# Optimization experiments

Hardware: AMD Instinct MI355X
Metric: run time of the kernel (lower is better)

## Reference

```python
import jax, jax.numpy as jnp
import numpy as np

N, C, H, W = 4, 256, 64, 64
OC = C // 8  # reduction=8

def setup_inputs() -> dict:
    key = jax.random.key(0)
    ks = jax.random.split(key, 5)
    return {
        "x": jax.random.normal(ks[0], (N, C, H, W), jnp.float32),
        "w1": jax.random.normal(ks[1], (OC, C), jnp.float32) * 0.05,
        "w2": jax.random.normal(ks[2], (OC, C), jnp.float32) * 0.05,
        "wv": jax.random.normal(ks[3], (C, C), jnp.float32) * 0.05,
        "scale": jax.random.normal(ks[4], (1,), jnp.float32),
    }

def reference(x, w1, w2, wv, scale):
    n, c, h, w = x.shape
    hw = h * w
    xf = x.reshape(n, c, hw)                      # (n, c, hw)
    r1 = jnp.einsum('oc,nci->noi', w1, xf)        # (n, oc, hw)  conv_reduce1
    r2 = jnp.einsum('oc,nci->noi', w2, xf)        # (n, oc, hw)  conv_reduce2
    # reduce_1^T @ reduce_2 -> (n, hw, hw); softmax over last dim (dim=2)
    A = jax.nn.softmax(jnp.einsum('noi,noj->nij', r1, r2), axis=2)
    v = jnp.einsum('oc,nci->noi', wv, xf)         # (n, c, hw)   value proj
    attn = jnp.einsum('nci,nij->ncj', v, A)       # (n, c, hw)
    return x + (scale[0] * attn).reshape(n, c, h, w)
```

## Files before the change

### kernel.cpp

```cpp
#include <hip/hip_runtime.h>
#include <math.h>

#define HW    4096
#define NCH   256
#define NB    4
#define L2E   1.44269504088896340736f

typedef __attribute__((ext_vector_type(8))) short short8b;
typedef __attribute__((ext_vector_type(4))) float f32x4;

__device__ __forceinline__ unsigned short f2bf(float f) {
    unsigned int u = __float_as_uint(f);
    u += 0x7FFFu + ((u >> 16) & 1u);
    return (unsigned short)(u >> 16);
}
__device__ __forceinline__ float bf2f(unsigned short h) {
    return __uint_as_float(((unsigned int)h) << 16);
}
__device__ __forceinline__ unsigned int cvtpk_bf16(float a, float b) {
    unsigned int r;
    asm("v_cvt_pk_bf16_f32 %0, %1, %2" : "=v"(r) : "v"(a), "v"(b));
    return r;
}


__global__ __launch_bounds__(256) void proj_rr_kernel(
    const float* __restrict__ x, const float* __restrict__ w1,
    const float* __restrict__ w2,
    unsigned short* __restrict__ r1h, unsigned short* __restrict__ r1l,
    unsigned short* __restrict__ r2h, unsigned short* __restrict__ r2l)
{
    __shared__ float aT[16][36];
    __shared__ float bS[16][68];

    const int t  = threadIdx.x;
    const int i0 = blockIdx.x * 64;
    const int mh = blockIdx.y * 32;
    const int n  = blockIdx.z;

    const int tm = t >> 4;
    const int ti = t & 15;

    const int ar = t >> 3;
    const int ak = (t & 7) * 2;
    const int gm = mh + ar;
    const float* arow = (gm < 32) ? (w1 + (size_t)gm * NCH)
                                  : (w2 + (size_t)(gm - 32) * NCH);
    const float* xb = x + (size_t)n * NCH * HW;

    float acc[2][4] = {};

    for (int kc = 0; kc < NCH; kc += 16) {
        float2 av = *reinterpret_cast<const float2*>(arow + kc + ak);
        float4 bv = *reinterpret_cast<const float4*>(
            xb + (size_t)(kc + (t >> 4)) * HW + i0 + (t & 15) * 4);
        __syncthreads();
        aT[ak + 0][ar] = av.x;
        aT[ak + 1][ar] = av.y;
        *reinterpret_cast<float4*>(&bS[t >> 4][(t & 15) * 4]) = bv;
        __syncthreads();
        #pragma unroll
        for (int kk = 0; kk < 16; ++kk) {
            float2 a2 = *reinterpret_cast<const float2*>(&aT[kk][tm * 2]);
            float4 b4 = *reinterpret_cast<const float4*>(&bS[kk][ti * 4]);
            float a[2] = {a2.x, a2.y};
            float b[4] = {b4.x, b4.y, b4.z, b4.w};
            #pragma unroll
            for (int mm = 0; mm < 2; ++mm)
                #pragma unroll
                for (int jj = 0; jj < 4; ++jj)
                    acc[mm][jj] = fmaf(a[mm], b[jj], acc[mm][jj]);
        }
    }

    #pragma unroll
    for (int mm = 0; mm < 2; ++mm) {
        const int m = mh + tm * 2 + mm;
        unsigned short* bhp = (m < 32) ? r1h : r2h;
        unsigned short* blp = (m < 32) ? r1l : r2l;
        const int o = m & 31;
        #pragma unroll
        for (int jj = 0; jj < 4; ++jj) {
            const int i = i0 + ti * 4 + jj;
            float v = acc[mm][jj];
            unsigned short h = f2bf(v);
            unsigned short lo = f2bf(v - bf2f(h));
            size_t idx = ((size_t)n * HW + i) * 32 + o;
            bhp[idx] = h;
            blp[idx] = lo;
        }
    }
}

__global__ __launch_bounds__(256) void wvb_kernel(
    const float* __restrict__ wv, unsigned short* __restrict__ wvb)
{
    const int q = (blockIdx.x * 256 + threadIdx.x) * 8;
    float4 a = *reinterpret_cast<const float4*>(wv + q);
    float4 b = *reinterpret_cast<const float4*>(wv + q + 4);
    short8b o;
    o[0] = (short)f2bf(a.x); o[1] = (short)f2bf(a.y);
    o[2] = (short)f2bf(a.z); o[3] = (short)f2bf(a.w);
    o[4] = (short)f2bf(b.x); o[5] = (short)f2bf(b.y);
    o[6] = (short)f2bf(b.z); o[7] = (short)f2bf(b.w);
    *reinterpret_cast<short8b*>(wvb + q) = o;
}

__global__ __launch_bounds__(256) void proj_v_kernel(
    const float* __restrict__ x, const unsigned short* __restrict__ wvb,
    unsigned short* __restrict__ vtb)
{
    __shared__ unsigned short xt[64][40];

    const int t = threadIdx.x;
    const int w = t >> 6, l = t & 63;
    const int lj = l & 15, lg = l >> 4;
    const int iB = blockIdx.x * 64;
    const int cB = blockIdx.y * 64;
    const int n  = blockIdx.z;
    const float* xb = x + (size_t)n * NCH * HW;

    const int iw = (w >> 1) * 32;
    const int cw = (w & 1) * 32;

    f32x4 acc[2][2] = {};

    const int kr = t >> 4;
    const int ic = (t & 15) * 4;

    for (int kc = 0; kc < NCH; kc += 32) {
        float4 x0 = *reinterpret_cast<const float4*>(
            xb + (size_t)(kc + kr) * HW + iB + ic);
        float4 x1 = *reinterpret_cast<const float4*>(
            xb + (size_t)(kc + kr + 16) * HW + iB + ic);
        __syncthreads();
        xt[ic + 0][kr] = f2bf(x0.x); xt[ic + 1][kr] = f2bf(x0.y);
        xt[ic + 2][kr] = f2bf(x0.z); xt[ic + 3][kr] = f2bf(x0.w);
        xt[ic + 0][kr + 16] = f2bf(x1.x); xt[ic + 1][kr + 16] = f2bf(x1.y);
        xt[ic + 2][kr + 16] = f2bf(x1.z); xt[ic + 3][kr + 16] = f2bf(x1.w);
        __syncthreads();

        short8b xa[2], wb[2];
        #pragma unroll
        for (int is = 0; is < 2; ++is)
            xa[is] = *reinterpret_cast<const short8b*>(&xt[iw + is * 16 + lj][lg * 8]);
        #pragma unroll
        for (int cs = 0; cs < 2; ++cs)
            wb[cs] = *reinterpret_cast<const short8b*>(
                wvb + (size_t)(cB + cw + cs * 16 + lj) * NCH + kc + lg * 8);
        #pragma unroll
        for (int is = 0; is < 2; ++is)
            #pragma unroll
            for (int cs = 0; cs < 2; ++cs)
                acc[is][cs] = __builtin_amdgcn_mfma_f32_16x16x32_bf16(
                    xa[is], wb[cs], acc[is][cs], 0, 0, 0);
    }

    unsigned short* op = vtb + (size_t)n * HW * 256;
    #pragma unroll
    for (int is = 0; is < 2; ++is) {
        #pragma unroll
        for (int cs = 0; cs < 2; ++cs) {
            const int c = cB + cw + cs * 16 + lj;
            #pragma unroll
            for (int r = 0; r < 4; ++r) {
                const int i = iB + iw + is * 16 + lg * 4 + r;
                op[(size_t)(i >> 5) * 8192 + c * 32 + (i & 31)] =
                    f2bf(acc[is][cs][r]);
            }
        }
    }
}

__global__ __launch_bounds__(256) void stats_kernel(
    const unsigned short* __restrict__ r1h, const unsigned short* __restrict__ r1l,
    const unsigned short* __restrict__ r2h, const unsigned short* __restrict__ r2l,
    float* __restrict__ mpart, float* __restrict__ lpart)
{
    const int t = threadIdx.x;
    const int w = t >> 6, l = t & 63;
    const int lj = l & 15, lg = l >> 4;
    const int i0 = blockIdx.x * 64 + w * 16;
    const int jh = blockIdx.y * 1024;
    const int n  = blockIdx.z;
    const size_t nHW = (size_t)n * HW;

    const size_t ab = (nHW + i0 + lj) * 32 + lg * 8;
    const short8b ah = *reinterpret_cast<const short8b*>(r1h + ab);
    const short8b al = *reinterpret_cast<const short8b*>(r1l + ab);
    const size_t bbase = (nHW + jh + lj) * 32 + lg * 8;

    f32x4 mx = {-INFINITY, -INFINITY, -INFINITY, -INFINITY};
    {
        short8b bh = *reinterpret_cast<const short8b*>(r2h + bbase);
        for (int jt = 0; jt < 64; ++jt) {
            short8b nh = bh;
            if (jt < 63)
                nh = *reinterpret_cast<const short8b*>(r2h + bbase + (size_t)(jt + 1) * 512);
            f32x4 s = {0.f, 0.f, 0.f, 0.f};
            s = __builtin_amdgcn_mfma_f32_16x16x32_bf16(ah, bh, s, 0, 0, 0);
            #pragma unroll
            for (int r = 0; r < 4; ++r) mx[r] = fmaxf(mx[r], s[r]);
            bh = nh;
        }
    }
    #pragma unroll
    for (int msk = 1; msk < 16; msk <<= 1)
        #pragma unroll
        for (int r = 0; r < 4; ++r)
            mx[r] = fmaxf(mx[r], __shfl_xor(mx[r], msk, 64));

    f32x4 sm = {0.f, 0.f, 0.f, 0.f};
    {
        short8b bh = *reinterpret_cast<const short8b*>(r2h + bbase);
        short8b bl = *reinterpret_cast<const short8b*>(r2l + bbase);
        for (int jt = 0; jt < 64; ++jt) {
            short8b nh = bh, nl = bl;
            if (jt < 63) {
                nh = *reinterpret_cast<const short8b*>(r2h + bbase + (size_t)(jt + 1) * 512);
                nl = *reinterpret_cast<const short8b*>(r2l + bbase + (size_t)(jt + 1) * 512);
            }
            f32x4 s = {0.f, 0.f, 0.f, 0.f};
            s = __builtin_amdgcn_mfma_f32_16x16x32_bf16(al, bh, s, 0, 0, 0);
            s = __builtin_amdgcn_mfma_f32_16x16x32_bf16(ah, bl, s, 0, 0, 0);
            s = __builtin_amdgcn_mfma_f32_16x16x32_bf16(ah, bh, s, 0, 0, 0);
            #pragma unroll
            for (int r = 0; r < 4; ++r) sm[r] += __expf(s[r] - mx[r]);
            bh = nh; bl = nl;
        }
    }
    #pragma unroll
    for (int msk = 1; msk < 16; msk <<= 1)
        #pragma unroll
        for (int r = 0; r < 4; ++r)
            sm[r] += __shfl_xor(sm[r], msk, 64);

    if (lj == 0) {
        float* mp = mpart + ((size_t)blockIdx.y * NB + n) * HW + i0 + lg * 4;
        float* lp = lpart + ((size_t)blockIdx.y * NB + n) * HW + i0 + lg * 4;
        #pragma unroll
        for (int r = 0; r < 4; ++r) { mp[r] = mx[r]; lp[r] = sm[r]; }
    }
}

__global__ __launch_bounds__(256) void merge_kernel(
    const float* __restrict__ mpart, const float* __restrict__ lpart,
    float* __restrict__ ebuf)
{
    const int q = blockIdx.x * 256 + threadIdx.x;
    const int T = NB * HW;
    float m0 = mpart[q], m1 = mpart[T + q];
    float m2 = mpart[2 * T + q], m3 = mpart[3 * T + q];
    float m = fmaxf(fmaxf(m0, m1), fmaxf(m2, m3));
    float lsum = lpart[q]         * __expf(m0 - m)
               + lpart[T + q]     * __expf(m1 - m)
               + lpart[2 * T + q] * __expf(m2 - m)
               + lpart[3 * T + q] * __expf(m3 - m);
    ebuf[q] = -m * L2E - log2f(lsum);
}

__global__ __launch_bounds__(512) void attn_kernel(
    const unsigned short* __restrict__ r1h, const unsigned short* __restrict__ r1l,
    const unsigned short* __restrict__ r2h, const unsigned short* __restrict__ r2l,
    const float* __restrict__ ebuf, const unsigned short* __restrict__ vtb,
    const float* __restrict__ x, const float* __restrict__ scale,
    float* __restrict__ out)
{
    __shared__ char pl[2][4096];

    const int t = threadIdx.x;
    const int w = t >> 6, l = t & 63;
    const int lj = l & 15, lg = l >> 4;

    const int bid = blockIdx.x;
    const int xcd = bid & 7;
    const int n   = xcd >> 1;
    const int j0  = ((xcd & 1) * 64 + (bid >> 3)) * 32;
    const size_t nHW = (size_t)n * HW;

    const int iw = w & 3;
    const int jw = w >> 2;

    const size_t rb = (nHW + j0 + jw * 16 + lj) * 32 + lg * 8;
    const short8b bh = *reinterpret_cast<const short8b*>(r2h + rb);
    const short8b bl = *reinterpret_cast<const short8b*>(r2l + rb);

    const unsigned short* vtn = vtb + nHW * 256;
    const int swz = (lj & 7) << 4;
    const int wroff = (jw * 16 + lj) * 128 + ((iw * 32 + lg * 8) ^ swz);
    int rdo[2][2];
    #pragma unroll
    for (int jf = 0; jf < 2; ++jf)
        #pragma unroll
        for (int ks = 0; ks < 2; ++ks)
            rdo[jf][ks] = (jf * 16 + lj) * 128 + ((ks * 64 + lg * 16) ^ swz);
    const size_t vrow = (size_t)(w * 32 + lj) * 32 + lg * 8;

    const float* erow = ebuf + nHW + iw * 16 + lg * 4;

    size_t abase = (nHW + iw * 16 + lj) * 32 + lg * 8;
    short8b ah = *reinterpret_cast<const short8b*>(r1h + abase);
    short8b al = *reinterpret_cast<const short8b*>(r1l + abase);
    float4 e4 = *reinterpret_cast<const float4*>(erow);
    {
        f32x4 s = {0.f, 0.f, 0.f, 0.f};
        s = __builtin_amdgcn_mfma_f32_16x16x32_bf16(al, bh, s, 0, 0, 0);
        s = __builtin_amdgcn_mfma_f32_16x16x32_bf16(ah, bl, s, 0, 0, 0);
        s = __builtin_amdgcn_mfma_f32_16x16x32_bf16(ah, bh, s, 0, 0, 0);
        float p0 = __builtin_amdgcn_exp2f(fmaf(s[0], L2E, e4.x));
        float p1 = __builtin_amdgcn_exp2f(fmaf(s[1], L2E, e4.y));
        float p2 = __builtin_amdgcn_exp2f(fmaf(s[2], L2E, e4.z));
        float p3 = __builtin_amdgcn_exp2f(fmaf(s[3], L2E, e4.w));
        *reinterpret_cast<uint2*>(&pl[0][wroff]) =
            make_uint2(cvtpk_bf16(p0, p1), cvtpk_bf16(p2, p3));
    }
    abase += 64 * 32;
    ah = *reinterpret_cast<const short8b*>(r1h + abase);
    al = *reinterpret_cast<const short8b*>(r1l + abase);
    e4 = *reinterpret_cast<const float4*>(erow + 64);
    __syncthreads();

    f32x4 acc[2][2] = {};

    for (int it = 0; it < 64; ++it) {
        const unsigned short* vb = vtn + (size_t)(it * 2) * 8192 + vrow;
        short8b va[2][2];
        #pragma unroll
        for (int cf = 0; cf < 2; ++cf)
            #pragma unroll
            for (int ks = 0; ks < 2; ++ks)
                va[cf][ks] = *reinterpret_cast<const short8b*>(
                    vb + cf * 512 + ks * 8192);

        if (it < 63) {
            f32x4 s = {0.f, 0.f, 0.f, 0.f};
            s = __builtin_amdgcn_mfma_f32_16x16x32_bf16(al, bh, s, 0, 0, 0);
            s = __builtin_amdgcn_mfma_f32_16x16x32_bf16(ah, bl, s, 0, 0, 0);
            s = __builtin_amdgcn_mfma_f32_16x16x32_bf16(ah, bh, s, 0, 0, 0);
            float p0 = __builtin_amdgcn_exp2f(fmaf(s[0], L2E, e4.x));
            float p1 = __builtin_amdgcn_exp2f(fmaf(s[1], L2E, e4.y));
            float p2 = __builtin_amdgcn_exp2f(fmaf(s[2], L2E, e4.z));
            float p3 = __builtin_amdgcn_exp2f(fmaf(s[3], L2E, e4.w));
            *reinterpret_cast<uint2*>(&pl[(it + 1) & 1][wroff]) =
                make_uint2(cvtpk_bf16(p0, p1), cvtpk_bf16(p2, p3));
            if (it < 62) {
                abase += 64 * 32;
                ah = *reinterpret_cast<const short8b*>(r1h + abase);
                al = *reinterpret_cast<const short8b*>(r1l + abase);
                e4 = *reinterpret_cast<const float4*>(erow + (it + 2) * 64);
            }
        }

        short8b pb[2][2];
        #pragma unroll
        for (int jf = 0; jf < 2; ++jf)
            #pragma unroll
            for (int ks = 0; ks < 2; ++ks)
                pb[jf][ks] = *reinterpret_cast<const short8b*>(
                    &pl[it & 1][rdo[jf][ks]]);
        #pragma unroll
        for (int cf = 0; cf < 2; ++cf)
            #pragma unroll
            for (int jf = 0; jf < 2; ++jf) {
                acc[cf][jf] = __builtin_amdgcn_mfma_f32_16x16x32_bf16(
                    va[cf][0], pb[jf][0], acc[cf][jf], 0, 0, 0);
                acc[cf][jf] = __builtin_amdgcn_mfma_f32_16x16x32_bf16(
                    va[cf][1], pb[jf][1], acc[cf][jf], 0, 0, 0);
            }
        __syncthreads();
    }

    const float sc = scale[0];
    const float* xb = x   + nHW * NCH;
    float*       ob = out + nHW * NCH;
    #pragma unroll
    for (int cf = 0; cf < 2; ++cf) {
        #pragma unroll
        for (int jf = 0; jf < 2; ++jf) {
            const int cb = w * 32 + cf * 16 + lg * 4;
            const int j  = j0 + jf * 16 + lj;
            #pragma unroll
            for (int r = 0; r < 4; ++r) {
                size_t off = (size_t)(cb + r) * HW + j;
                ob[off] = xb[off] + sc * acc[cf][jf][r];
            }
        }
    }
}

extern "C" void kernel_launch(void* const* d_in, const int* in_sizes, int n_in,
                              void* d_out, int out_size, void* d_ws, size_t ws_size,
                              hipStream_t stream) {
    (void)in_sizes; (void)n_in; (void)out_size; (void)ws_size;
    const float* x  = (const float*)d_in[0];
    const float* w1 = (const float*)d_in[1];
    const float* w2 = (const float*)d_in[2];
    const float* wv = (const float*)d_in[3];
    const float* sc = (const float*)d_in[4];
    float* out = (float*)d_out;

    float* ebuf  = (float*)d_ws;
    float* spare = ebuf + (size_t)NB * HW;
    unsigned short* r1h = (unsigned short*)(spare + (size_t)NB * HW);
    unsigned short* r1l = r1h + (size_t)NB * HW * 32;
    unsigned short* r2h = r1l + (size_t)NB * HW * 32;
    unsigned short* r2l = r2h + (size_t)NB * HW * 32;
    unsigned short* vtb = r2l + (size_t)NB * HW * 32;
    unsigned short* wvb = vtb + (size_t)NB * HW * 256;
    float* mpart = (float*)vtb;
    float* lpart = mpart + (size_t)4 * NB * HW;

    proj_rr_kernel<<<dim3(64, 2, NB), 256, 0, stream>>>(x, w1, w2,
                                                        r1h, r1l, r2h, r2l);
    stats_kernel<<<dim3(64, 4, NB), 256, 0, stream>>>(r1h, r1l, r2h, r2l,
                                                      mpart, lpart);
    merge_kernel<<<dim3(NB * HW / 256), 256, 0, stream>>>(mpart, lpart, ebuf);
    wvb_kernel<<<dim3(32), 256, 0, stream>>>(wv, wvb);
    proj_v_kernel<<<dim3(64, 4, NB), 256, 0, stream>>>(x, wvb, vtb);
    attn_kernel<<<dim3(512), 512, 0, stream>>>(
        r1h, r1l, r2h, r2l, ebuf, vtb, x, sc, out);
}
```

Before: 181.2 us.

## Use single-pass online softmax stats and retile attention to 16-column blocks

The stats kernel now makes one pass over r2 with an online max/sum in base-2, where it used to run a separate max pass followed by a sum pass, and the cross-lane reduction merges (max, sum) pairs. The attention kernel moves from 512-thread blocks covering 32 output columns to 256-thread blocks covering 16 columns, launched as twice as many blocks. Each wave now handles 64 channels with 4 accumulators, and s_setprio is raised around the MFMA section. Halving the stats loads of r2 and giving the attention kernel more, smaller blocks should cut memory traffic and raise occupancy, at the cost of recomputing the attention scores in twice as many blocks.

Result: slower. 222.0 us (+22.5%).

```diff
diff --git a/kernel.cpp b/kernel.cpp
--- a/kernel.cpp
+++ b/kernel.cpp
@@ -191,49 +191,43 @@
     const size_t bbase = (nHW + jh + lj) * 32 + lg * 8;
 
     f32x4 mx = {-INFINITY, -INFINITY, -INFINITY, -INFINITY};
-    {
-        short8b bh = *reinterpret_cast<const short8b*>(r2h + bbase);
-        for (int jt = 0; jt < 64; ++jt) {
-            short8b nh = bh;
-            if (jt < 63)
-                nh = *reinterpret_cast<const short8b*>(r2h + bbase + (size_t)(jt + 1) * 512);
-            f32x4 s = {0.f, 0.f, 0.f, 0.f};
-            s = __builtin_amdgcn_mfma_f32_16x16x32_bf16(ah, bh, s, 0, 0, 0);
-            #pragma unroll
-            for (int r = 0; r < 4; ++r) mx[r] = fmaxf(mx[r], s[r]);
-            bh = nh;
-        }
-    }
+    f32x4 sm = {0.f, 0.f, 0.f, 0.f};
+
+    short8b bh = *reinterpret_cast<const short8b*>(r2h + bbase);
+    short8b bl = *reinterpret_cast<const short8b*>(r2l + bbase);
+    for (int jt = 0; jt < 64; ++jt) {
+        short8b nh = bh, nl = bl;
+        if (jt < 63) {
+            nh = *reinterpret_cast<const short8b*>(r2h + bbase + (size_t)(jt + 1) * 512);
+            nl = *reinterpret_cast<const short8b*>(r2l + bbase + (size_t)(jt + 1) * 512);
+        }
+        f32x4 s = {0.f, 0.f, 0.f, 0.f};
+        s = __builtin_amdgcn_mfma_f32_16x16x32_bf16(al, bh, s, 0, 0, 0);
+        s = __builtin_amdgcn_mfma_f32_16x16x32_bf16(ah, bl, s, 0, 0, 0);
+        s = __builtin_amdgcn_mfma_f32_16x16x32_bf16(ah, bh, s, 0, 0, 0);
+        #pragma unroll
+        for (int r = 0; r < 4; ++r) {
+            float s2 = s[r] * L2E;
+            float mn = fmaxf(mx[r], s2);
+            sm[r] = fmaf(sm[r], __builtin_amdgcn_exp2f(mx[r] - mn),
+                         __builtin_amdgcn_exp2f(s2 - mn));
+            mx[r] = mn;
+        }
+        bh = nh; bl = nl;
+    }
+
     #pragma unroll
-    for (int msk = 1; msk < 16; msk <<= 1)
-        #pragma unroll
-        for (int r = 0; r < 4; ++r)
-            mx[r] = fmaxf(mx[r], __shfl_xor(mx[r], msk, 64));
-
-    f32x4 sm = {0.f, 0.f, 0.f, 0.f};
-    {
-        short8b bh = *reinterpret_cast<const short8b*>(r2h + bbase);
-        short8b bl = *reinterpret_cast<const short8b*>(r2l + bbase);
-        for (int jt = 0; jt < 64; ++jt) {
-            short8b nh = bh, nl = bl;
-            if (jt < 63) {
-                nh = *reinterpret_cast<const short8b*>(r2h + bbase + (size_t)(jt + 1) * 512);
-                nl = *reinterpret_cast<const short8b*>(r2l + bbase + (size_t)(jt + 1) * 512);
-            }
-            f32x4 s = {0.f, 0.f, 0.f, 0.f};
-            s = __builtin_amdgcn_mfma_f32_16x16x32_bf16(al, bh, s, 0, 0, 0);
-            s = __builtin_amdgcn_mfma_f32_16x16x32_bf16(ah, bl, s, 0, 0, 0);
-            s = __builtin_amdgcn_mfma_f32_16x16x32_bf16(ah, bh, s, 0, 0, 0);
-            #pragma unroll
-            for (int r = 0; r < 4; ++r) sm[r] += __expf(s[r] - mx[r]);
-            bh = nh; bl = nl;
-        }
-    }
-    #pragma unroll
-    for (int msk = 1; msk < 16; msk <<= 1)
-        #pragma unroll
-        for (int r = 0; r < 4; ++r)
-            sm[r] += __shfl_xor(sm[r], msk, 64);
+    for (int msk = 1; msk < 16; msk <<= 1) {
+        #pragma unroll
+        for (int r = 0; r < 4; ++r) {
+            float mo = __shfl_xor(mx[r], msk, 64);
+            float so = __shfl_xor(sm[r], msk, 64);
+            float mn = fmaxf(mx[r], mo);
+            sm[r] = sm[r] * __builtin_amdgcn_exp2f(mx[r] - mn)
+                  + so    * __builtin_amdgcn_exp2f(mo    - mn);
+            mx[r] = mn;
+        }
+    }
 
     if (lj == 0) {
         float* mp = mpart + ((size_t)blockIdx.y * NB + n) * HW + i0 + lg * 4;
@@ -252,21 +246,21 @@
     float m0 = mpart[q], m1 = mpart[T + q];
     float m2 = mpart[2 * T + q], m3 = mpart[3 * T + q];
     float m = fmaxf(fmaxf(m0, m1), fmaxf(m2, m3));
-    float lsum = lpart[q]         * __expf(m0 - m)
-               + lpart[T + q]     * __expf(m1 - m)
-               + lpart[2 * T + q] * __expf(m2 - m)
-               + lpart[3 * T + q] * __expf(m3 - m);
-    ebuf[q] = -m * L2E - log2f(lsum);
-}
-
-__global__ __launch_bounds__(512) void attn_kernel(
+    float lsum = lpart[q]         * __builtin_amdgcn_exp2f(m0 - m)
+               + lpart[T + q]     * __builtin_amdgcn_exp2f(m1 - m)
+               + lpart[2 * T + q] * __builtin_amdgcn_exp2f(m2 - m)
+               + lpart[3 * T + q] * __builtin_amdgcn_exp2f(m3 - m);
+    ebuf[q] = -m - log2f(lsum);
+}
+
+__global__ __launch_bounds__(256) void attn_kernel(
     const unsigned short* __restrict__ r1h, const unsigned short* __restrict__ r1l,
     const unsigned short* __restrict__ r2h, const unsigned short* __restrict__ r2l,
     const float* __restrict__ ebuf, const unsigned short* __restrict__ vtb,
     const float* __restrict__ x, const float* __restrict__ scale,
     float* __restrict__ out)
 {
-    __shared__ char pl[2][4096];
+    __shared__ char pl[2][2048];
 
     const int t = threadIdx.x;
     const int w = t >> 6, l = t & 63;
@@ -275,30 +269,22 @@
     const int bid = blockIdx.x;
     const int xcd = bid & 7;
     const int n   = xcd >> 1;
-    const int j0  = ((xcd & 1) * 64 + (bid >> 3)) * 32;
+    const int j0  = (xcd & 1) * 2048 + (bid >> 3) * 16;
     const size_t nHW = (size_t)n * HW;
 
-    const int iw = w & 3;
-    const int jw = w >> 2;
-
-    const size_t rb = (nHW + j0 + jw * 16 + lj) * 32 + lg * 8;
+    const size_t rb = (nHW + j0 + lj) * 32 + lg * 8;
     const short8b bh = *reinterpret_cast<const short8b*>(r2h + rb);
     const short8b bl = *reinterpret_cast<const short8b*>(r2l + rb);
 
     const unsigned short* vtn = vtb + nHW * 256;
     const int swz = (lj & 7) << 4;
-    const int wroff = (jw * 16 + lj) * 128 + ((iw * 32 + lg * 8) ^ swz);
-    int rdo[2][2];
-    #pragma unroll
-    for (int jf = 0; jf < 2; ++jf)
-        #pragma unroll
-        for (int ks = 0; ks < 2; ++ks)
-            rdo[jf][ks] = (jf * 16 + lj) * 128 + ((ks * 64 + lg * 16) ^ swz);
-    const size_t vrow = (size_t)(w * 32 + lj) * 32 + lg * 8;
-
-    const float* erow = ebuf + nHW + iw * 16 + lg * 4;
-
-    size_t abase = (nHW + iw * 16 + lj) * 32 + lg * 8;
+    const int wroff = lj * 128 + ((w * 32 + lg * 8) ^ swz);
+    const int rd0 = lj * 128 + ((lg * 16) ^ swz);
+    const int rd1 = lj * 128 + ((64 + lg * 16) ^ swz);
+    const size_t vrow = (size_t)(w * 64 + lj) * 32 + lg * 8;
+    const float* erow = ebuf + nHW + w * 16 + lg * 4;
+
+    size_t abase = (nHW + w * 16 + lj) * 32 + lg * 8;
     short8b ah = *reinterpret_cast<const short8b*>(r1h + abase);
     short8b al = *reinterpret_cast<const short8b*>(r1l + abase);
     float4 e4 = *reinterpret_cast<const float4*>(erow);
@@ -314,19 +300,19 @@
         *reinterpret_cast<uint2*>(&pl[0][wroff]) =
             make_uint2(cvtpk_bf16(p0, p1), cvtpk_bf16(p2, p3));
     }
-    abase += 64 * 32;
+    abase += 2048;
     ah = *reinterpret_cast<const short8b*>(r1h + abase);
     al = *reinterpret_cast<const short8b*>(r1l + abase);
     e4 = *reinterpret_cast<const float4*>(erow + 64);
     __syncthreads();
 
-    f32x4 acc[2][2] = {};
+    f32x4 acc[4] = {};
 
     for (int it = 0; it < 64; ++it) {
         const unsigned short* vb = vtn + (size_t)(it * 2) * 8192 + vrow;
-        short8b va[2][2];
-        #pragma unroll
-        for (int cf = 0; cf < 2; ++cf)
+        short8b va[4][2];
+        #pragma unroll
+        for (int cf = 0; cf < 4; ++cf)
             #pragma unroll
             for (int ks = 0; ks < 2; ++ks)
                 va[cf][ks] = *reinterpret_cast<const short8b*>(
@@ -344,29 +330,24 @@
             *reinterpret_cast<uint2*>(&pl[(it + 1) & 1][wroff]) =
                 make_uint2(cvtpk_bf16(p0, p1), cvtpk_bf16(p2, p3));
             if (it < 62) {
-                abase += 64 * 32;
+                abase += 2048;
                 ah = *reinterpret_cast<const short8b*>(r1h + abase);
                 al = *reinterpret_cast<const short8b*>(r1l + abase);
                 e4 = *reinterpret_cast<const float4*>(erow + (it + 2) * 64);
             }
         }
 
-        short8b pb[2][2];
-        #pragma unroll
-        for (int jf = 0; jf < 2; ++jf)
-            #pragma unroll
-            for (int ks = 0; ks < 2; ++ks)
-                pb[jf][ks] = *reinterpret_cast<const short8b*>(
-                    &pl[it & 1][rdo[jf][ks]]);
-        #pragma unroll
-        for (int cf = 0; cf < 2; ++cf)
-            #pragma unroll
-            for (int jf = 0; jf < 2; ++jf) {
-                acc[cf][jf] = __builtin_amdgcn_mfma_f32_16x16x32_bf16(
-                    va[cf][0], pb[jf][0], acc[cf][jf], 0, 0, 0);
-                acc[cf][jf] = __builtin_amdgcn_mfma_f32_16x16x32_bf16(
-                    va[cf][1], pb[jf][1], acc[cf][jf], 0, 0, 0);
-            }
+        short8b pb0 = *reinterpret_cast<const short8b*>(&pl[it & 1][rd0]);
+        short8b pb1 = *reinterpret_cast<const short8b*>(&pl[it & 1][rd1]);
+        __builtin_amdgcn_s_setprio(1);
+        #pragma unroll
+        for (int cf = 0; cf < 4; ++cf) {
+            acc[cf] = __builtin_amdgcn_mfma_f32_16x16x32_bf16(
+                va[cf][0], pb0, acc[cf], 0, 0, 0);
+            acc[cf] = __builtin_amdgcn_mfma_f32_16x16x32_bf16(
+                va[cf][1], pb1, acc[cf], 0, 0, 0);
+        }
+        __builtin_amdgcn_s_setprio(0);
         __syncthreads();
     }
 
@@ -374,16 +355,12 @@
     const float* xb = x   + nHW * NCH;
     float*       ob = out + nHW * NCH;
     #pragma unroll
-    for (int cf = 0; cf < 2; ++cf) {
-        #pragma unroll
-        for (int jf = 0; jf < 2; ++jf) {
-            const int cb = w * 32 + cf * 16 + lg * 4;
-            const int j  = j0 + jf * 16 + lj;
-            #pragma unroll
-            for (int r = 0; r < 4; ++r) {
-                size_t off = (size_t)(cb + r) * HW + j;
-                ob[off] = xb[off] + sc * acc[cf][jf][r];
-            }
+    for (int cf = 0; cf < 4; ++cf) {
+        const int cb = w * 64 + cf * 16 + lg * 4;
+        #pragma unroll
+        for (int r = 0; r < 4; ++r) {
+            size_t off = (size_t)(cb + r) * HW + j0 + lj;
+            ob[off] = xb[off] + sc * acc[cf][r];
         }
     }
 }
@@ -417,6 +394,6 @@
     merge_kernel<<<dim3(NB * HW / 256), 256, 0, stream>>>(mpart, lpart, ebuf);
     wvb_kernel<<<dim3(32), 256, 0, stream>>>(wv, wvb);
     proj_v_kernel<<<dim3(64, 4, NB), 256, 0, stream>>>(x, wvb, vtb);
-    attn_kernel<<<dim3(512), 512, 0, stream>>>(
+    attn_kernel<<<dim3(1024), 256, 0, stream>>>(
         r1h, r1l, r2h, r2l, ebuf, vtb, x, sc, out);
 }
```
